# Optimization experiments

Hardware: AMD Instinct MI355X
Metric: run time of the kernel (lower is better)

Reference implementation:

```python
import jax, jax.numpy as jnp
import numpy as np
from jax.scipy.special import logsumexp

B, T, LD, HD, K = 64, 2048, 16, 64, 8
TEMP = 1.0  # annealing=False
LOG2PI = float(np.log(2.0 * np.pi))


def setup_inputs() -> dict:
    key = jax.random.key(0)
    ks = jax.random.split(key, 10)
    return {
        "z": jax.random.normal(ks[0], (B, T, LD), jnp.float32),
        "pi": jax.random.normal(ks[1], (K,), jnp.float32) * 0.5,
        "Q": jax.random.normal(ks[2], (K, K), jnp.float32) * 0.5,
        "init_mean": jax.random.normal(ks[3], (K, LD), jnp.float32),
        # torch init: rand(K,1,1) * eye(LD) * 5  (a scale factor per state)
        "init_cov": jax.random.uniform(ks[4], (K, 1, 1), jnp.float32) * 5.0 * jnp.eye(LD, dtype=jnp.float32)[None],
        "covs": jnp.tile(jnp.eye(LD, dtype=jnp.float32)[None], (K, 1, 1)) + 0.05 * jax.random.normal(ks[5], (K, LD, LD), jnp.float32),
        "W1": jax.random.normal(ks[6], (K, HD, LD), jnp.float32) / np.sqrt(LD),
        "b1": jnp.zeros((K, HD), jnp.float32),
        "W2": jax.random.normal(ks[7], (K, LD, HD), jnp.float32) / np.sqrt(HD),
        "b2": jnp.zeros((K, LD), jnp.float32),
    }


def _chol_terms(C):
    """Sigma = C C^T + 1e-6 I ; return (L^{-1}, 0.5*logdet) per state."""
    dim = C.shape[-1]
    Sigma = C @ jnp.swapaxes(C, -1, -2) + 1e-6 * jnp.eye(dim, dtype=C.dtype)
    L = jnp.linalg.cholesky(Sigma)  # [K,D,D]
    Linv = jax.vmap(lambda l: jax.scipy.linalg.solve_triangular(l, jnp.eye(dim, dtype=C.dtype), lower=True))(L)
    logdet_half = jnp.sum(jnp.log(jnp.diagonal(L, axis1=-2, axis2=-1)), -1)  # [K]
    return Linv, logdet_half


def _mvn_logp(diff, Linv, logdet_half):
    # diff [B,t,K,D], Linv [K,D,D] -> [B,t,K]
    y = jnp.einsum('kde,btke->btkd', Linv, diff)
    maha = jnp.sum(y * y, -1)
    d = diff.shape[-1]
    return -0.5 * maha - logdet_half - 0.5 * d * LOG2PI


def reference(z, pi, Q, init_mean, init_cov, covs, W1, b1, W2, b2):
    # ---- local evidence: log p(z_1|s_1), log p(z_t | z_{t-1}, s_t)  [B,T,K]
    Linv0, ld0 = _chol_terms(init_cov)
    le1 = _mvn_logp(z[:, :1, None, :] - init_mean, Linv0, ld0)  # [B,1,K]
    zp = z[:, :-1]  # [B,T-1,D]
    h = jax.nn.softplus(jnp.einsum('btd,khd->btkh', zp, W1) + b1)  # per-state MLP hidden
    mu = jnp.einsum('btkh,kdh->btkd', h, W2) + b2  # [B,T-1,K,D]
    LinvT, ldT = _chol_terms(covs)
    leT = _mvn_logp(z[:, 1:, None, :] - mu, LinvT, ldT)  # [B,T-1,K]
    le = jnp.concatenate([le1, leT], axis=1)  # [B,T,K]

    # ---- alpha recursion (filtering)
    logpi = jax.nn.log_softmax(pi / TEMP)
    Qlog = jax.nn.log_softmax(Q / TEMP, axis=-1)  # log p(s_t=j | s_{t-1}=i)
    QT = Qlog.T  # [to, from]
    lp0 = le[:, 0] + logpi
    lz0 = logsumexp(lp0, -1)
    la0 = lp0 - lz0[:, None]
    le_rest = jnp.swapaxes(le[:, 1:], 0, 1)  # [T-1,B,K]

    def astep(la_prev, le_t):
        lp = logsumexp(le_t[:, :, None] + QT[None] + la_prev[:, None, :], axis=-1)
        lz = logsumexp(lp, -1)
        la = lp - lz[:, None]
        return la, (la, lz)

    _, (las, lzs) = jax.lax.scan(astep, la0, le_rest)
    log_alpha = jnp.concatenate([la0[:, None], jnp.swapaxes(las, 0, 1)], axis=1)  # [B,T,K]
    log_Z = jnp.concatenate([lz0[:, None], lzs.T], axis=1)  # [B,T]

    # ---- beta recursion (smoothing), reverse scan
    def bstep(lb_next, inp):
        le_t, lz_t = inp
        lb = logsumexp(Qlog[None] + le_t[:, None, :] + lb_next[:, None, :], axis=-1) - lz_t[:, None]
        return lb, lb

    _, lbs = jax.lax.scan(bstep, jnp.zeros((B, K), le.dtype), (le_rest, log_Z[:, 1:].T), reverse=True)
    log_beta = jnp.concatenate([jnp.swapaxes(lbs, 0, 1), jnp.zeros((B, 1, K), le.dtype)], axis=1)

    # ---- posteriors
    gamma = jnp.exp(log_alpha + log_beta)  # [B,T,K]
    paired = jnp.exp(Qlog[None, None] + log_alpha[:, :-1, :, None] + log_beta[:, 1:, None, :] + le[:, 1:, None, :] - log_Z[:, 1:, None, None])  # [B,T-1,K,K]
    return gamma, paired, log_Z
```

## Files before the change

### kernel.cpp

```cpp
#include <hip/hip_runtime.h>

#define B_ 64
#define T_ 2048
#define LD_ 16
#define HD_ 64
#define K_ 8
#define L_ 8
#define C_ 256
#define S_ 32

constexpr int OFF_LE    = 0;
constexpr int OFF_ALPHA = 1048576;
constexpr int OFF_ZT    = OFF_ALPHA;
constexpr int OFF_SBUF  = 2097152;
constexpr int OFF_UBUF  = 2228224;
constexpr int OFF_RLOG  = 2359296;
constexpr int OFF_ULOG  = 2375680;
constexpr int OFF_SAIN  = 2377728;
constexpr int OFF_BENT  = 2394112;
constexpr int OFF_PBUF  = 2410496;
constexpr int OFF_PRML  = 3459072;
constexpr int OFF_FRAG  = 3463680;

constexpr int P_LINV0 = 0;
constexpr int P_LINVT = 2048;
constexpr int P_LD0   = 4096;
constexpr int P_LDT   = 4104;
constexpr int P_LOGPI = 4112;

constexpr int FI_NC2 = 32768;
constexpr int FI_C0I = 32896;

constexpr int OUT_PAIRED = B_*T_*K_;
constexpr int OUT_LOGZ   = OUT_PAIRED + B_*(T_-1)*K_*K_;

template<int CTRL>
__device__ __forceinline__ float dppmov(float x) {
  int xi = __float_as_int(x);
  int r = __builtin_amdgcn_update_dpp(xi, xi, CTRL, 0xF, 0xF, true);
  return __int_as_float(r);
}
__device__ __forceinline__ void allg8(float v, float w[8]) {
  w[0] = v;
  w[1] = dppmov<0xB1>(v);
  w[2] = dppmov<0x4E>(v);
  w[3] = dppmov<0x4E>(w[1]);
  w[7] = dppmov<0x141>(v);
  w[6] = dppmov<0xB1>(w[7]);
  w[5] = dppmov<0x4E>(w[7]);
  w[4] = dppmov<0x4E>(w[6]);
}
template<int V> __device__ __forceinline__ float xorg8(float x);
template<> __device__ __forceinline__ float xorg8<0>(float x) { return x; }
template<> __device__ __forceinline__ float xorg8<1>(float x) { return dppmov<0xB1>(x); }
template<> __device__ __forceinline__ float xorg8<2>(float x) { return dppmov<0x4E>(x); }
template<> __device__ __forceinline__ float xorg8<3>(float x) { return dppmov<0x4E>(dppmov<0xB1>(x)); }
template<> __device__ __forceinline__ float xorg8<4>(float x) { return dppmov<0x4E>(dppmov<0xB1>(dppmov<0x141>(x))); }
template<> __device__ __forceinline__ float xorg8<5>(float x) { return dppmov<0x4E>(dppmov<0x141>(x)); }
// ... 22 lines not shown
  w[7] = __int_as_float(__builtin_amdgcn_ds_swizzle(x, 0xF8));
}
__device__ __forceinline__ void col2row(const float cl[8], float rv[8]) {
  rv[0] = cl[0];
  rv[1] = xorg8<1>(cl[1]);
  rv[2] = xorg8<2>(cl[2]);
  rv[3] = xorg8<3>(cl[3]);
  rv[4] = xorg8<4>(cl[4]);
  rv[5] = xorg8<5>(cl[5]);
  rv[6] = xorg8<6>(cl[6]);
  rv[7] = xorg8<7>(cl[7]);
}
__device__ __forceinline__ void mmul8(const float a[8], const float m[8], float o[8]) {
  float m8[8][8];
  #pragma unroll
  for (int w = 0; w < 8; w++) allg8(m[w], m8[w]);
  #pragma unroll
  for (int v = 0; v < 8; v++) {
    float acc = 0.f;
    #pragma unroll
    for (int u = 0; u < 8; u++) acc = __builtin_fmaf(a[u], m8[u^v][u], acc);
    o[v] = acc;
  }
}
__device__ __forceinline__ float maxnorm8(float m[8]) {
  float mx = m[0];
  #pragma unroll
  for (int u = 1; u < 8; u++) mx = fmaxf(mx, m[u]);
  mx = bfly_max8(mx);
  float r = rcpnr(mx);
  #pragma unroll
  for (int u = 0; u < 8; u++) m[u] *= r;
  return mx;
}
__device__ __forceinline__ void load_rows(const float* p, float r[8]) {
  const float4* q = (const float4*)p;
  float4 x0 = q[0], x1 = q[1];
  r[0]=x0.x; r[1]=x0.y; r[2]=x0.z; r[3]=x0.w;
  r[4]=x1.x; r[5]=x1.y; r[6]=x1.z; r[7]=x1.w;
}
__device__ __forceinline__ float dotw8(const float r[8], const float w[8]) {
  return ((r[0]*w[0]+r[1]*w[1]) + (r[2]*w[2]+r[3]*w[3]))
       + ((r[4]*w[4]+r[5]*w[5]) + (r[6]*w[6]+r[7]*w[7]));
}
__device__ __forceinline__ void fill_Qe(const float* __restrict__ Qm, float* Qe) {
  if (threadIdx.x < 8) {
    int r = threadIdx.x;
    float qq[8], mx = -1e30f;
    #pragma unroll
    for (int c2 = 0; c2 < 8; c2++) { qq[c2] = Qm[r*8+c2]; mx = fmaxf(mx, qq[c2]); }
    float s = 0.f;
    #pragma unroll
    for (int c2 = 0; c2 < 8; c2++) s += __expf(qq[c2]-mx);
    float ls = __logf(s);
    #pragma unroll
    for (int c2 = 0; c2 < 8; c2++) Qe[r*8+c2] = __expf(qq[c2]-mx-ls);
  }
}

typedef __attribute__((ext_vector_type(4))) float f32x4;
typedef __attribute__((ext_vector_type(8))) short bf16x8;

__device__ __forceinline__ unsigned ph(float a, float b) {
  return (__float_as_uint(a) >> 16) | (__float_as_uint(b) & 0xFFFF0000u);
}
__device__ __forceinline__ float hif(float a) {
  return __uint_as_float(__float_as_uint(a) & 0xFFFF0000u);
}
__device__ __forceinline__ bf16x8 u2f(uint4 u) {
  return __builtin_bit_cast(bf16x8, u);
}
__device__ __forceinline__ uint4 mkfrag_u4(float4 v) {
  unsigned ux = __float_as_uint(v.x), uy = __float_as_uint(v.y);
  unsigned uz = __float_as_uint(v.z), uw = __float_as_uint(v.w);
  unsigned h01 = (ux >> 16) | (uy & 0xFFFF0000u);
  unsigned h23 = (uz >> 16) | (uw & 0xFFFF0000u);
  float lx = v.x - __uint_as_float(ux & 0xFFFF0000u);
  float ly = v.y - __uint_as_float(uy & 0xFFFF0000u);
  float lz = v.z - __uint_as_float(uz & 0xFFFF0000u);
  float lw = v.w - __uint_as_float(uw & 0xFFFF0000u);
  return make_uint4(h01, h23, ph(lx,ly), ph(lz,lw));
}
__device__ __forceinline__ f32x4 MF(bf16x8 a, bf16x8 b, f32x4 c) {
  return __builtin_amdgcn_mfma_f32_16x16x32_bf16(a, b, c, 0, 0, 0);
}

__global__ __launch_bounds__(64) void prep_kernel(
    const float* __restrict__ pi, const float* __restrict__ Q,
    const float* __restrict__ init_cov, const float* __restrict__ covs,
    float* __restrict__ prm)
{
  int tid = threadIdx.x;
  int blk = blockIdx.x;
  if (blk < 16) {
    int k = blk & 7;
    const float* C = (blk < 8 ? init_cov : covs) + k*256;
    float* outL  = prm + (blk < 8 ? P_LINV0 : P_LINVT) + k*256;
    float* outld = prm + (blk < 8 ? P_LD0   : P_LDT)   + k;
    __shared__ float S[16][17], L[16][17], X[16][17];
    for (int e = tid; e < 256; e += 64) {
      int r = e >> 4, c = e & 15;
      float s = (r == c) ? 1e-6f : 0.f;
      for (int l = 0; l < 16; l++) s += C[r*16+l] * C[c*16+l];
      S[r][c] = s;
    }
    __syncthreads();
    for (int j = 0; j < 16; j++) {
      if (tid == 0) L[j][j] = sqrtf(S[j][j]);
      __syncthreads();
      if (tid > j && tid < 16) L[tid][j] = S[tid][j] / L[j][j];
      __syncthreads();
      if (tid > j && tid < 16) {
        float ltj = L[tid][j];
        for (int c = j+1; c <= tid; c++) S[tid][c] -= ltj * L[c][j];
      }
      __syncthreads();
    }
    if (tid < 16) {
      int c = tid;
      for (int r = 0; r < 16; r++) {
        float v;
        if (r < c) v = 0.f;
        else {
          v = (r == c) ? 1.f : 0.f;
          for (int s2 = c; s2 < r; s2++) v -= L[r][s2] * X[s2][c];
          v /= L[r][r];
        }
        X[r][c] = v;
      }
    }
    __syncthreads();
    for (int e = tid; e < 256; e += 64) outL[e] = X[e>>4][e&15];
    if (tid == 0) {
      float ld = 0.f;
      for (int j = 0; j < 16; j++) ld += logf(L[j][j]);
      *outld = ld;
    }
  } else {
    if (tid == 0) {
      float p[8], mx = -1e30f;
      for (int j = 0; j < 8; j++) { p[j] = pi[j]; mx = fmaxf(mx, p[j]); }
      float s = 0.f;
      for (int j = 0; j < 8; j++) s += __expf(p[j]-mx);
      float ls = logf(s);
      for (int j = 0; j < 8; j++) prm[P_LOGPI+j] = p[j]-mx-ls;
    }
  }
}

__global__ __launch_bounds__(64) void prep2_kernel(
    const float* __restrict__ W1, const float* __restrict__ W2,
    const float* __restrict__ b2, const float* __restrict__ init_mean,
    const float* __restrict__ prm, float* __restrict__ frag)
{
  int k = blockIdx.x, tid = threadIdx.x;
  __shared__ float Ls[16][16], L0s[16][16], G[16][64];
  for (int e = tid; e < 256; e += 64) {
    Ls[e>>4][e&15]  = prm[P_LINVT + k*256 + e];
    L0s[e>>4][e&15] = prm[P_LINV0 + k*256 + e];
  }
  __syncthreads();
  for (int idx = tid; idx < 1024; idx += 64) {
    int d = idx >> 6, hh = idx & 63;
    float s = 0.f;
    for (int e = 0; e < 16; e++) s += Ls[d][e] * W2[k*1024 + e*64 + hh];
    G[d][hh] = -s;
  }
  __syncthreads();
  int d = tid & 15, q = tid >> 4;
  uint4* F4 = (uint4*)frag;
  for (int kc = 0; kc < 2; kc++) {
    float v[8], lo[8];
    for (int j = 0; j < 8; j++) {
      int hh = 32*kc + 16*(j>>2) + 4*q + (j&3);
      v[j] = G[d][hh];
      lo[j] = v[j] - hif(v[j]);
    }
    F4[6144 + ((k*2+kc)*4+q)*16 + d] =
        make_uint4(ph(v[0],v[1]), ph(v[2],v[3]), ph(v[4],v[5]), ph(v[6],v[7]));
    F4[7168 + ((k*2+kc)*4+q)*16 + d] =
        make_uint4(ph(lo[0],lo[1]), ph(lo[2],lo[3]), ph(lo[4],lo[5]), ph(lo[6],lo[7]));
  }
  for (int mt = 0; mt < 4; mt++) {
    int hh = 16*mt + d;
    float v[4], lo[4];
    for (int j = 0; j < 4; j++) { v[j] = W1[k*1024 + hh*16 + 4*q + j]; lo[j] = v[j] - hif(v[j]); }
    unsigned x = ph(v[0],v[1]), y = ph(v[2],v[3]);
    F4[((k*4+mt)*4+q)*16 + d]        = make_uint4(x, y, x, y);
    F4[2048 + ((k*4+mt)*4+q)*16 + d] = make_uint4(ph(lo[0],lo[1]), ph(lo[2],lo[3]), 0u, 0u);
  }
  {
    float v[4], lo[4];
    for (int j = 0; j < 4; j++) { v[j] = Ls[d][4*q+j]; lo[j] = v[j] - hif(v[j]); }
    unsigned x = ph(v[0],v[1]), y = ph(v[2],v[3]);
    F4[4096 + (k*4+q)*16 + d] = make_uint4(x, y, x, y);
    F4[4608 + (k*4+q)*16 + d] = make_uint4(ph(lo[0],lo[1]), ph(lo[2],lo[3]), 0u, 0u);
    for (int j = 0; j < 4; j++) { v[j] = L0s[d][4*q+j]; lo[j] = v[j] - hif(v[j]); }
    x = ph(v[0],v[1]); y = ph(v[2],v[3]);
    F4[5120 + (k*4+q)*16 + d] = make_uint4(x, y, x, y);
    F4[5632 + (k*4+q)*16 + d] = make_uint4(ph(lo[0],lo[1]), ph(lo[2],lo[3]), 0u, 0u);
  }
  if (q == 0) {
    float s2 = 0.f, s0 = 0.f;
    for (int e = 0; e < 16; e++) {
      s2 += Ls[d][e]  * b2[k*16+e];
      s0 += L0s[d][e] * init_mean[k*16+e];
    }
    frag[FI_NC2 + k*16 + d] = -s2;
    frag[FI_C0I + k*16 + d] = -s0;
  }
}

__global__ __launch_bounds__(256) void ztr_kernel(
    const float* __restrict__ z, uint4* __restrict__ zf)
{
  int tid = blockIdx.x*256 + threadIdx.x;
  int t = tid >> 6, b = tid & 63;
  const float4* src = (const float4*)(z + (b*T_ + t)*LD_);
  #pragma unroll
  for (int q = 0; q < 4; q++)
    zf[(t*4 + q)*64 + b] = mkfrag_u4(src[q]);
}

__global__ __launch_bounds__(256) void emisB_kernel(
    const uint4* __restrict__ zf, const float* __restrict__ b1,
    const float* __restrict__ frag, const float* __restrict__ prm,
    float* __restrict__ lebuf)
{
  int lane = threadIdx.x & 63;
  int wid = __builtin_amdgcn_readfirstlane(blockIdx.x*4 + (threadIdx.x >> 6));
  int bblk = wid & 3;
  int tch  = (wid >> 2) & 255;
  int k    = wid >> 10;
  int c = lane & 15, q = lane >> 4;
  int b = bblk*16 + c;
  const uint4* F4 = (const uint4*)frag;

  bf16x8 w1a1[4], w1a2[4];
  #pragma unroll
  for (int mt = 0; mt < 4; mt++) {
    w1a1[mt] = u2f(F4[((k*4+mt)*4+q)*16 + c]);
    w1a2[mt] = u2f(F4[2048 + ((k*4+mt)*4+q)*16 + c]);
// ... 3 lines not shown
  bf16x8 gahi[2], galo[2];
  #pragma unroll
  for (int kc = 0; kc < 2; kc++) {
    gahi[kc] = u2f(F4[6144 + ((k*2+kc)*4+q)*16 + c]);
    galo[kc] = u2f(F4[7168 + ((k*2+kc)*4+q)*16 + c]);
  }
  float b1iv[16];
  #pragma unroll
  for (int i = 0; i < 16; i++)
    b1iv[i] = b1[k*64 + (i>>2)*16 + 4*q + (i&3)];
  float nc2[4];
  #pragma unroll
  for (int r = 0; r < 4; r++) nc2[r] = frag[FI_NC2 + k*16 + 4*q + r];
  float lconst = -prm[P_LDT + k] - 14.70301653f;

  int t0 = tch*8;
  bf16x8 zp;
  int ttstart;
  if (tch == 0) {
    bf16x8 zc0 = u2f(zf[q*64 + b]);
    bf16x8 l0a1 = u2f(F4[5120 + (k*4+q)*16 + c]);
    bf16x8 l0a2 = u2f(F4[5632 + (k*4+q)*16 + c]);
    f32x4 acc;
    acc[0] = frag[FI_C0I + k*16 + 4*q + 0];
    acc[1] = frag[FI_C0I + k*16 + 4*q + 1];
    acc[2] = frag[FI_C0I + k*16 + 4*q + 2];
    acc[3] = frag[FI_C0I + k*16 + 4*q + 3];
    acc = MF(l0a1, zc0, acc);
    acc = MF(l0a2, zc0, acc);
    float m2 = (acc[0]*acc[0] + acc[1]*acc[1]) + (acc[2]*acc[2] + acc[3]*acc[3]);
    m2 += __shfl_xor(m2, 16);
    m2 += __shfl_xor(m2, 32);
    float le = -0.5f*m2 - prm[P_LD0+k] - 14.70301653f + prm[P_LOGPI+k];
    if (q == 0) lebuf[k*64 + b] = le;
    zp = zc0;
    ttstart = 1;
  } else {
    zp = u2f(zf[((t0-1)*4 + q)*64 + b]);
    ttstart = 0;
  }

  uint4 zvu = zf[((t0+ttstart)*4 + q)*64 + b];
  #pragma unroll 1
  for (int tt = ttstart; tt < 8; tt++) {
    int t = t0 + tt;
    uint4 zvn = zvu;
    if (tt < 7) zvn = zf[((t+1)*4 + q)*64 + b];
    bf16x8 zc = u2f(zvu);
    f32x4 a1[4];
    #pragma unroll
    for (int mt = 0; mt < 4; mt++) {
      f32x4 ai;
      ai[0] = b1iv[mt*4+0]; ai[1] = b1iv[mt*4+1];
      ai[2] = b1iv[mt*4+2]; ai[3] = b1iv[mt*4+3];
      ai = MF(w1a1[mt], zp, ai);
      a1[mt] = MF(w1a2[mt], zp, ai);
    }
    float hv[16];
    #pragma unroll
    for (int i = 0; i < 16; i++) {
      float a = a1[i>>2][i&3];
      hv[i] = __logf(1.f + __expf(a));
    }
    bf16x8 hhi[2], hlo[2];
    #pragma unroll
    for (int kc = 0; kc < 2; kc++) {
      const float* hp = hv + 8*kc;
      hhi[kc] = u2f(make_uint4(ph(hp[0],hp[1]), ph(hp[2],hp[3]),
                               ph(hp[4],hp[5]), ph(hp[6],hp[7])));
      float l0 = hp[0]-hif(hp[0]), l1 = hp[1]-hif(hp[1]);
      float l2 = hp[2]-hif(hp[2]), l3 = hp[3]-hif(hp[3]);
      float l4 = hp[4]-hif(hp[4]), l5 = hp[5]-hif(hp[5]);
      float l6 = hp[6]-hif(hp[6]), l7 = hp[7]-hif(hp[7]);
      hlo[kc] = u2f(make_uint4(ph(l0,l1), ph(l2,l3), ph(l4,l5), ph(l6,l7)));
    }
    f32x4 acc;
    acc[0] = nc2[0]; acc[1] = nc2[1]; acc[2] = nc2[2]; acc[3] = nc2[3];
    acc = MF(lva1, zc, acc);
    acc = MF(lva2, zc, acc);
    #pragma unroll
    for (int kc = 0; kc < 2; kc++) {
      acc = MF(gahi[kc], hhi[kc], acc);
      acc = MF(galo[kc], hhi[kc], acc);
      acc = MF(gahi[kc], hlo[kc], acc);
    }
    float m2 = (acc[0]*acc[0] + acc[1]*acc[1]) + (acc[2]*acc[2] + acc[3]*acc[3]);
    m2 += __shfl_xor(m2, 16);
    m2 += __shfl_xor(m2, 32);
    float le = -0.5f*m2 + lconst;
    if (q == 0) lebuf[t*512 + k*64 + b] = le;
    zp = zc;
    zvu = zvn;
  }
}

__global__ __launch_bounds__(256) void fwdA_kernel(
    const float* __restrict__ lebuf, const float* __restrict__ Qm,
    float* __restrict__ pbuf, float* __restrict__ sbuf)
{
  __shared__ float Qe[64];
  __shared__ float M[4][8][64];
  fill_Qe(Qm, Qe);
  int lane64 = threadIdx.x & 63;
  int iu = threadIdx.x >> 6;
  int unit = blockIdx.x*4 + iu;
  int b = unit & 63, s = unit >> 6;
  int u = lane64 >> 3, j = lane64 & 7;
  int c = 8*s + u;
  float lev[8];
  #pragma unroll
  for (int x = 0; x < 8; x++) lev[x] = lebuf[(c*L_+x)*512 + j*64 + b];
  __syncthreads();
  float qtv[64];
  #pragma unroll
  for (int x = 0; x < 8; x++)
    #pragma unroll
    for (int v = 0; v < 8; v++)
      qtv[x*8+v] = Qe[(j^v)*8 + (j^x)];
  float pl[8];
  if (c == 0) {
    float m = bfly_max8(lev[0]);
    float e = __expf(lev[0]-m);
    allg8(e, pl);
  } else {
    float m = bfly_max8(lev[0]);
    float e = __expf(lev[0]-m);
    float e8[8]; allg8(e, e8);
    float np[8];
    #pragma unroll
    for (int x = 0; x < 8; x++) np[x] = e8[x] * qtv[x*8];
    float mx = np[0];
    #pragma unroll
    for (int x = 1; x < 8; x++) mx = fmaxf(mx, np[x]);
    mx = bfly_max8(mx);
    float r = rcpnr(mx);
    #pragma unroll
    for (int x = 0; x < 8; x++) pl[x] = np[x] * r;
  }
  #pragma unroll
  for (int sx = 1; sx < 8; sx++) {
    float m = bfly_max8(lev[sx]);
    float e = __expf(lev[sx]-m);
    float e8[8]; allg8(e, e8);
    float np[8];
    #pragma unroll
    for (int x = 0; x < 8; x++) {
      float acc = 0.f;
      #pragma unroll
      for (int v = 0; v < 8; v++) acc = __builtin_fmaf(qtv[x*8+v], pl[v], acc);
      np[x] = e8[x] * acc;
    }
    float mx = np[0];
    #pragma unroll
    for (int x = 1; x < 8; x++) mx = fmaxf(mx, np[x]);
    mx = bfly_max8(mx);
    float r = rcpnr(mx);
    #pragma unroll
    for (int x = 0; x < 8; x++) pl[x] = np[x] * r;
  }
  float rv[8]; col2row(pl, rv);
  float4* dst = (float4*)(pbuf + (c*64 + b)*64 + j*8);
  dst[0] = make_float4(rv[0], rv[1], rv[2], rv[3]);
  dst[1] = make_float4(rv[4], rv[5], rv[6], rv[7]);
  #pragma unroll
  for (int v = 0; v < 8; v++) M[iu][u][j*8+v] = rv[v];
  __syncthreads();
  if (u == 0) {
    float m[8];
    #pragma unroll
    for (int v = 0; v < 8; v++) m[v] = M[iu][0][j*8+v];
    for (int cc = 1; cc < 8; cc++) {
      float a[8];
      #pragma unroll
      for (int v = 0; v < 8; v++) a[v] = M[iu][cc][j*8+v];
      float nm[8];
      mmul8(a, m, nm);
      maxnorm8(nm);
      #pragma unroll
      for (int v = 0; v < 8; v++) m[v] = nm[v];
    }
    float4* d2 = (float4*)(sbuf + (s*64 + b)*64 + j*8);
    d2[0] = make_float4(m[0], m[1], m[2], m[3]);
    d2[1] = make_float4(m[4], m[5], m[6], m[7]);
  }
}

__global__ __launch_bounds__(512) void fwdP2b_kernel(
    const float* __restrict__ sbuf, float* __restrict__ sain)
{
  int lane = threadIdx.x;
  int b = lane >> 3, i = lane & 7;
  const float4* base = (const float4*)sbuf;
  float4 c0 = base[(0*64+b)*16 + i*2], c1 = base[(0*64+b)*16 + i*2 + 1];
  float a = 0.125f;
  for (int s = 0; s < S_; s++) {
    int s2 = (s < S_-1) ? s+1 : S_-1;
    float4 n0 = base[(s2*64+b)*16 + i*2], n1 = base[(s2*64+b)*16 + i*2 + 1];
    float aw[8]; allg8(a, aw);
    float sm = ((c0.x*aw[0] + c0.y*aw[1]) + (c0.z*aw[2] + c0.w*aw[3]))
             + ((c1.x*aw[4] + c1.y*aw[5]) + (c1.z*aw[6] + c1.w*aw[7]));
    float tot = bfly_sum8(sm);
    float an = sm * rcpnr(tot);
    if (s < S_-1) { a = an; sain[(s+1)*512 + b*8 + i] = a; }
    c0 = n0; c1 = n1;
  }
}

__global__ __launch_bounds__(256) void fwdB_kernel(
    const float* __restrict__ lebuf, const float* __restrict__ Qm,
    const float* __restrict__ sain, float* pbuf,
    float* __restrict__ alpha, float* __restrict__ rlog,
    float* __restrict__ ubuf, float* __restrict__ ulog,
    float* __restrict__ out)
{
  __shared__ float Qe[64];
  __shared__ float Als[4][8];
  __shared__ float Mh[4][8][64];
  __shared__ float Lh[4][8];
  fill_Qe(Qm, Qe);
  int lane64 = threadIdx.x & 63;
  int iu = threadIdx.x >> 6;
  int unit = blockIdx.x*4 + iu;
  int b = unit & 63, s = unit >> 6;
  int u = lane64 >> 3, i = lane64 & 7;
  int c = 8*s + u;
  int off = b*8 + i;
  float pr[8];
  load_rows(pbuf + (c*64 + b)*64 + i*8, pr);
  float lev[8];
  #pragma unroll
  for (int x = 0; x < 8; x++) lev[x] = lebuf[(c*L_+x)*512 + i*64 + b];
  __syncthreads();
  float q[8];
  #pragma unroll
  for (int x = 0; x < 8; x++) q[x] = Qe[(i^x)*8 + i];
  float av_in = 0.f;
  if (u == 0) av_in = (s == 0) ? 0.125f : sain[s*512 + off];
  for (int r = 0; r < 7; r++) {
    if (u == r) {
      if (r > 0) av_in = Als[iu][i];
      float aw[8]; allg8(av_in, aw);
      float sm = dotw8(pr, aw);
      float tot = bfly_sum8(sm);
      Als[iu][i] = sm * rcpnr(tot);
    }
    __syncthreads();
  }
  if (u == 7) av_in = Als[iu][i];
  float* logZ = out + OUT_LOGZ + b*T_;
  float eb_loc[8];
  float a;
  if (c == 0) {
    float m0 = bfly_max8(lev[0]);
    float e0x = __expf(lev[0]-m0);
    float ct = bfly_sum8(e0x);
    float rr = rcpnr(ct);
    a = e0x * rr;
    alpha[off] = a;
    eb_loc[0] = a;
    if (i == 0) logZ[0] = m0 + __logf(ct);
  } else {
    a = av_in;
    int t = c*L_;
    float m = bfly_max8(lev[0]);
    float e = __expf(lev[0]-m);
    float w[8]; allg8(a, w);
    float dot = dotw8(q, w);
    float p = e * dot;
    float ct = bfly_sum8(p);
    float rr = rcpnr(ct);
    a = p * rr;
    alpha[t*512 + off] = a;
    eb_loc[0] = e * rr;
    if (i == 0) logZ[t] = m + __logf(ct);
  }
  #pragma unroll
  for (int x = 1; x < 8; x++) {
    int t = c*L_ + x;
    float m = bfly_max8(lev[x]);
    float e = __expf(lev[x]-m);
    float w[8]; allg8(a, w);
    float dot = dotw8(q, w);
    float p = e * dot;
    float ct = bfly_sum8(p);
    float rr = rcpnr(ct);
    a = p * rr;
    alpha[t*512 + off] = a;
    eb_loc[x] = e * rr;
    if (i == 0) logZ[t] = m + __logf(ct);
  }
  float qv[64];
  #pragma unroll
  for (int x = 0; x < 8; x++)
    #pragma unroll
    for (int v = 0; v < 8; v++)
      qv[x*8+v] = Qe[(i^x)*8 + (i^v)];
  float rl8[8];
  #pragma unroll
  for (int x = 0; x < 8; x++) rl8[x] = (x == 0) ? 1.f : 0.f;
  float lsc = 0.f;
  #pragma unroll
  for (int sx = 7; sx >= 1; sx--) {
    float e8[8]; allg8(eb_loc[sx], e8);
    float nr[8];
    #pragma unroll
    for (int x = 0; x < 8; x++) {
      float acc = 0.f;
      #pragma unroll
      for (int v = 0; v < 8; v++) acc = __builtin_fmaf(qv[x*8+v], e8[v]*rl8[v], acc);
      nr[x] = acc;
    }
    float mx = nr[0];
    #pragma unroll
    for (int x = 1; x < 8; x++) mx = fmaxf(mx, nr[x]);
    mx = bfly_max8(mx);
    float r = rcpnr(mx);
    #pragma unroll
    for (int x = 0; x < 8; x++) rl8[x] = nr[x] * r;
    lsc += __logf(mx);
  }
  float rv[8]; col2row(rl8, rv);
  float4* dstR = (float4*)(pbuf + (c*64 + b)*64 + i*8);
  dstR[0] = make_float4(rv[0], rv[1], rv[2], rv[3]);
  dstR[1] = make_float4(rv[4], rv[5], rv[6], rv[7]);
  if (i == 0) rlog[c*64 + b] = lsc;
  float qr[8];
  #pragma unroll
  for (int x = 0; x < 8; x++) qr[x] = Qe[i*8 + (i^x)];
  float d8[8];
  #pragma unroll
  for (int v = 0; v < 8; v++) d8[v] = eb_loc[0] * rv[v];
  float h8[8];
  mmul8(qr, d8, h8);
  float ls = lsc + __logf(maxnorm8(h8));
  #pragma unroll
  for (int v = 0; v < 8; v++) Mh[iu][u][i*8+v] = h8[v];
  if (i == 0) Lh[iu][u] = ls;
  __syncthreads();
  if (u == 0) {
    float m[8];
    #pragma unroll
    for (int v = 0; v < 8; v++) m[v] = Mh[iu][7][i*8+v];
    float lsum = Lh[iu][7];
    for (int cc = 6; cc >= 0; cc--) {
      float aa[8];
      #pragma unroll
      for (int v = 0; v < 8; v++) aa[v] = Mh[iu][cc][i*8+v];
      float t8[8];
      mmul8(aa, m, t8);
      lsum += Lh[iu][cc] + __logf(maxnorm8(t8));
      #pragma unroll
      for (int v = 0; v < 8; v++) m[v] = t8[v];
    }
    float4* d2 = (float4*)(ubuf + (s*64 + b)*64 + i*8);
    d2[0] = make_float4(m[0], m[1], m[2], m[3]);
    d2[1] = make_float4(m[4], m[5], m[6], m[7]);
    if (i == 0) ulog[s*64 + b] = lsum;
  }
}

__global__ __launch_bounds__(512) void bwdP2b_kernel(
    const float* __restrict__ ubuf, const float* __restrict__ ulog,
    float* __restrict__ bent)
{
  int lane = threadIdx.x;
  int b = lane >> 3, i = lane & 7;
  bent[(S_-1)*512 + b*8 + i] = 1.f;
  const float4* base = (const float4*)ubuf;
  float sh = 1.f, sig = 0.f;
  float4 c0 = base[((S_-1)*64+b)*16 + i*2], c1 = base[((S_-1)*64+b)*16 + i*2 + 1];
  float cu = ulog[(S_-1)*64 + b];
  for (int s = S_-1; s >= 1; s--) {
    int s2 = (s > 1) ? s-1 : 1;
    float4 n0 = base[(s2*64+b)*16 + i*2], n1 = base[(s2*64+b)*16 + i*2 + 1];
    float nu = ulog[s2*64 + b];
    float sw[8]; allg8(sh, sw);
    float y = ((c0.x*sw[0] + c0.y*sw[1]) + (c0.z*sw[2] + c0.w*sw[3]))
            + ((c1.x*sw[4] + c1.y*sw[5]) + (c1.z*sw[6] + c1.w*sw[7]));
    float mx = bfly_max8(y);
    sh = y * rcpnr(mx);
    sig += cu + __logf(mx);
    bent[(s-1)*512 + b*8 + i] = sh * __expf(sig);
    c0 = n0; c1 = n1; cu = nu;
  }
}

__global__ __launch_bounds__(256) void bwdC_kernel(
    const float* __restrict__ alpha, const float* __restrict__ lebuf,
    const float* __restrict__ rbuf, const float* __restrict__ rlog,
    const float* __restrict__ Qm, const float* __restrict__ bent,
    float* __restrict__ out)
{
  __shared__ float Qe[64];
  __shared__ float Bls[4][8];
  fill_Qe(Qm, Qe);
  int lane64 = threadIdx.x & 63;
  int iu = threadIdx.x >> 6;
  int unit = blockIdx.x*4 + iu;
  int b = unit & 63, s = unit >> 6;
  int u = lane64 >> 3, i = lane64 & 7;
  int c = 8*s + u;
  int off = b*8 + i;
  float r8[8];
  load_rows(rbuf + (c*64 + b)*64 + i*8, r8);
  float erl = __expf(rlog[c*64 + b]);
  float av[8], lev[8];
  #pragma unroll
  for (int x = 0; x < 8; x++) av[x] = alpha[(c*L_+x)*512 + off];
  #pragma unroll
  for (int x = 0; x < 8; x++) lev[x] = lebuf[(c*L_+x)*512 + i*64 + b];
  const float* lzp = out + OUT_LOGZ + b*T_ + c*L_;
  float4 lz0 = *(const float4*)lzp;
  float4 lz1 = *(const float4*)(lzp + 4);
  float ev[8];
  ev[0] = __expf(lev[0]-lz0.x); ev[1] = __expf(lev[1]-lz0.y);
  ev[2] = __expf(lev[2]-lz0.z); ev[3] = __expf(lev[3]-lz0.w);
  ev[4] = __expf(lev[4]-lz1.x); ev[5] = __expf(lev[5]-lz1.y);
  ev[6] = __expf(lev[6]-lz1.z); ev[7] = __expf(lev[7]-lz1.w);
  float e0 = ev[0];
  float avm1 = (c > 0) ? alpha[(c*L_-1)*512 + off] : 0.f;
  __syncthreads();
  float qr[8], qa[8];
  #pragma unroll
  for (int x = 0; x < 8; x++) qr[x] = Qe[i*8 + (i^x)];
  #pragma unroll
  for (int v = 0; v < 8; v++) qa[v] = Qe[i*8 + v];
  float bt = 0.f, y = 0.f, nbv = 0.f;
  for (int r = 7; r >= 0; r--) {
    if (u == r) {
      bt = (r == 7) ? bent[s*512 + off] : Bls[iu][i];
      float bw[8]; allg8(bt, bw);
      y = dotw8(r8, bw) * erl;
      float ey = e0 * y;
      float w[8]; allg8(ey, w);
      nbv = 0.f;
      #pragma unroll
      for (int v = 0; v < 8; v++) nbv = __builtin_fmaf(qr[v], w[v], nbv);
      if (r > 0) Bls[iu][i] = nbv;
    }
    __syncthreads();
  }
  float* po = out + OUT_PAIRED + b*((T_-1)*64);
  float* go = out + b*(T_*K_);
  float bb = bt;
  if (c == C_-1) go[2047*8 + i] = av[7];
  #pragma unroll
  for (int x = 7; x >= 1; x--) {
    float eya[8]; absg8(ev[x]*bb, eya);
    float term[8];
    #pragma unroll
    for (int v = 0; v < 8; v++) term[v] = qa[v]*eya[v];
    float nb = ((term[0]+term[1]) + (term[2]+term[3]))
             + ((term[4]+term[5]) + (term[6]+term[7]));
    int t = c*L_ + x - 1;
    float am = av[x-1];
    float4* pd = (float4*)(po + t*64 + i*8);
    pd[0] = make_float4(am*term[0], am*term[1], am*term[2], am*term[3]);
    pd[1] = make_float4(am*term[4], am*term[5], am*term[6], am*term[7]);
    go[t*8 + i] = am*nb;
    bb = nb;
  }
  if (c > 0) {
    float eya[8]; absg8(e0*y, eya);
    int t = c*L_ - 1;
    float4* pd = (float4*)(po + t*64 + i*8);
    pd[0] = make_float4(avm1*qa[0]*eya[0], avm1*qa[1]*eya[1],
                        avm1*qa[2]*eya[2], avm1*qa[3]*eya[3]);
    pd[1] = make_float4(avm1*qa[4]*eya[4], avm1*qa[5]*eya[5],
                        avm1*qa[6]*eya[6], avm1*qa[7]*eya[7]);
    go[t*8 + i] = avm1 * nbv;
  }
}

extern "C" void kernel_launch(void* const* d_in, const int* in_sizes, int n_in,
                              void* d_out, int out_size, void* d_ws, size_t ws_size,
                              hipStream_t stream) {
  const float* z         = (const float*)d_in[0];
  const float* pi        = (const float*)d_in[1];
  const float* Q         = (const float*)d_in[2];
  const float* init_mean = (const float*)d_in[3];
  const float* init_cov  = (const float*)d_in[4];
  const float* covs      = (const float*)d_in[5];
  const float* W1        = (const float*)d_in[6];
  const float* b1        = (const float*)d_in[7];
  const float* W2        = (const float*)d_in[8];
  const float* b2        = (const float*)d_in[9];
  float* out = (float*)d_out;
  float* ws  = (float*)d_ws;

  prep_kernel<<<17, 64, 0, stream>>>(pi, Q, init_cov, covs, ws + OFF_PRML);
  prep2_kernel<<<8, 64, 0, stream>>>(W1, W2, b2, init_mean, ws + OFF_PRML,
                                     ws + OFF_FRAG);
  ztr_kernel<<<512, 256, 0, stream>>>(z, (uint4*)(ws + OFF_ZT));
  emisB_kernel<<<2048, 256, 0, stream>>>((const uint4*)(ws + OFF_ZT), b1,
                                         ws + OFF_FRAG, ws + OFF_PRML,
                                         ws + OFF_LE);
  fwdA_kernel<<<512, 256, 0, stream>>>(ws + OFF_LE, Q, ws + OFF_PBUF,
                                       ws + OFF_SBUF);
  fwdP2b_kernel<<<1, 512, 0, stream>>>(ws + OFF_SBUF, ws + OFF_SAIN);
  fwdB_kernel<<<512, 256, 0, stream>>>(ws + OFF_LE, Q, ws + OFF_SAIN,
                                       ws + OFF_PBUF, ws + OFF_ALPHA,
                                       ws + OFF_RLOG, ws + OFF_UBUF,
                                       ws + OFF_ULOG, out);
  bwdP2b_kernel<<<1, 512, 0, stream>>>(ws + OFF_UBUF, ws + OFF_ULOG,
                                       ws + OFF_BENT);
  bwdC_kernel<<<512, 256, 0, stream>>>(ws + OFF_ALPHA, ws + OFF_LE,
                                       ws + OFF_PBUF, ws + OFF_RLOG, Q,
                                       ws + OFF_BENT, out);
}
```

Before: 234.1 us.

## Halve chunk length, recompute chunk transfer matrices instead of staging through pbuf

Chunk length drops from 8 to 4 steps, so there are twice as many chunks and superchunks and the fwdA/fwdB/bwdC grids double. The per-chunk forward and backward transfer matrices are no longer written to and reloaded from a global pbuf/rlog buffer. fwdB and bwdC now recompute them locally from the emissions. The serial superchunk scan kernels become fully unrolled direct loads over a longer sequence of 64 steps. This trades global memory traffic and a longer serial pass for redundant in-register compute and more parallel work.

```diff
diff --git a/kernel.cpp b/kernel.cpp
--- a/kernel.cpp
+++ b/kernel.cpp
@@ -5,22 +5,20 @@
 #define LD_ 16
 #define HD_ 64
 #define K_ 8
-#define L_ 8
-#define C_ 256
-#define S_ 32
+#define L_ 4
+#define C_ 512
+#define S_ 64
 
 constexpr int OFF_LE    = 0;
 constexpr int OFF_ALPHA = 1048576;
 constexpr int OFF_ZT    = OFF_ALPHA;
 constexpr int OFF_SBUF  = 2097152;
-constexpr int OFF_UBUF  = 2228224;
-constexpr int OFF_RLOG  = 2359296;
-constexpr int OFF_ULOG  = 2375680;
-constexpr int OFF_SAIN  = 2377728;
-constexpr int OFF_BENT  = 2394112;
-constexpr int OFF_PBUF  = 2410496;
-constexpr int OFF_PRML  = 3459072;
-constexpr int OFF_FRAG  = 3463680;
+constexpr int OFF_UBUF  = 2359296;
+constexpr int OFF_ULOG  = 2621440;
+constexpr int OFF_SAIN  = 2625536;
+constexpr int OFF_BENT  = 2658304;
+constexpr int OFF_PRML  = 3145728;
+constexpr int OFF_FRAG  = 3150336;
 
 constexpr int P_LINV0 = 0;
 constexpr int P_LINVT = 2048;
@@ -112,12 +110,6 @@
   #pragma unroll
   for (int u = 0; u < 8; u++) m[u] *= r;
   return mx;
-}
-__device__ __forceinline__ void load_rows(const float* p, float r[8]) {
-  const float4* q = (const float4*)p;
-  float4 x0 = q[0], x1 = q[1];
-  r[0]=x0.x; r[1]=x0.y; r[2]=x0.z; r[3]=x0.w;
-  r[4]=x1.x; r[5]=x1.y; r[6]=x1.z; r[7]=x1.w;
 }
 __device__ __forceinline__ float dotw8(const float r[8], const float w[8]) {
   return ((r[0]*w[0]+r[1]*w[1]) + (r[2]*w[2]+r[3]*w[3]))
@@ -421,7 +413,7 @@
 
 __global__ __launch_bounds__(256) void fwdA_kernel(
     const float* __restrict__ lebuf, const float* __restrict__ Qm,
-    float* __restrict__ pbuf, float* __restrict__ sbuf)
+    float* __restrict__ sbuf)
 {
   __shared__ float Qe[64];
   __shared__ float M[4][8][64];
@@ -432,9 +424,9 @@
   int b = unit & 63, s = unit >> 6;
   int u = lane64 >> 3, j = lane64 & 7;
   int c = 8*s + u;
-  float lev[8];
-  #pragma unroll
-  for (int x = 0; x < 8; x++) lev[x] = lebuf[(c*L_+x)*512 + j*64 + b];
+  float lev[L_];
+  #pragma unroll
+  for (int x = 0; x < L_; x++) lev[x] = lebuf[(c*L_+x)*512 + j*64 + b];
   __syncthreads();
   float qtv[64];
   #pragma unroll
@@ -463,7 +455,7 @@
     for (int x = 0; x < 8; x++) pl[x] = np[x] * r;
   }
   #pragma unroll
-  for (int sx = 1; sx < 8; sx++) {
+  for (int sx = 1; sx < L_; sx++) {
     float m = bfly_max8(lev[sx]);
     float e = __expf(lev[sx]-m);
     float e8[8]; allg8(e, e8);
@@ -484,9 +476,6 @@
     for (int x = 0; x < 8; x++) pl[x] = np[x] * r;
   }
   float rv[8]; col2row(pl, rv);
-  float4* dst = (float4*)(pbuf + (c*64 + b)*64 + j*8);
-  dst[0] = make_float4(rv[0], rv[1], rv[2], rv[3]);
-  dst[1] = make_float4(rv[4], rv[5], rv[6], rv[7]);
   #pragma unroll
   for (int v = 0; v < 8; v++) M[iu][u][j*8+v] = rv[v];
   __syncthreads();
@@ -516,25 +505,23 @@
   int lane = threadIdx.x;
   int b = lane >> 3, i = lane & 7;
   const float4* base = (const float4*)sbuf;
-  float4 c0 = base[(0*64+b)*16 + i*2], c1 = base[(0*64+b)*16 + i*2 + 1];
   float a = 0.125f;
-  for (int s = 0; s < S_; s++) {
-    int s2 = (s < S_-1) ? s+1 : S_-1;
-    float4 n0 = base[(s2*64+b)*16 + i*2], n1 = base[(s2*64+b)*16 + i*2 + 1];
+  #pragma unroll
+  for (int s = 0; s < S_-1; s++) {
+    float4 c0 = base[(s*64+b)*16 + i*2];
+    float4 c1 = base[(s*64+b)*16 + i*2 + 1];
     float aw[8]; allg8(a, aw);
     float sm = ((c0.x*aw[0] + c0.y*aw[1]) + (c0.z*aw[2] + c0.w*aw[3]))
              + ((c1.x*aw[4] + c1.y*aw[5]) + (c1.z*aw[6] + c1.w*aw[7]));
     float tot = bfly_sum8(sm);
-    float an = sm * rcpnr(tot);
-    if (s < S_-1) { a = an; sain[(s+1)*512 + b*8 + i] = a; }
-    c0 = n0; c1 = n1;
+    a = sm * rcpnr(tot);
+    sain[(s+1)*512 + b*8 + i] = a;
   }
 }
 
 __global__ __launch_bounds__(256) void fwdB_kernel(
     const float* __restrict__ lebuf, const float* __restrict__ Qm,
-    const float* __restrict__ sain, float* pbuf,
-    float* __restrict__ alpha, float* __restrict__ rlog,
+    const float* __restrict__ sain, float* __restrict__ alpha,
     float* __restrict__ ubuf, float* __restrict__ ulog,
     float* __restrict__ out)
 {
@@ -550,15 +537,61 @@
   int u = lane64 >> 3, i = lane64 & 7;
   int c = 8*s + u;
   int off = b*8 + i;
+  float lev[L_];
+  #pragma unroll
+  for (int x = 0; x < L_; x++) lev[x] = lebuf[(c*L_+x)*512 + i*64 + b];
+  __syncthreads();
   float pr[8];
-  load_rows(pbuf + (c*64 + b)*64 + i*8, pr);
-  float lev[8];
-  #pragma unroll
-  for (int x = 0; x < 8; x++) lev[x] = lebuf[(c*L_+x)*512 + i*64 + b];
-  __syncthreads();
-  float q[8];
-  #pragma unroll
-  for (int x = 0; x < 8; x++) q[x] = Qe[(i^x)*8 + i];
+  {
+    float qtv[64];
+    #pragma unroll
+    for (int x = 0; x < 8; x++)
+      #pragma unroll
+      for (int v = 0; v < 8; v++)
+        qtv[x*8+v] = Qe[(i^v)*8 + (i^x)];
+    float pl[8];
+    if (c == 0) {
+      float m = bfly_max8(lev[0]);
+      float e = __expf(lev[0]-m);
+      allg8(e, pl);
+    } else {
+      float m = bfly_max8(lev[0]);
+      float e = __expf(lev[0]-m);
+      float e8[8]; allg8(e, e8);
+      float np[8];
+      #pragma unroll
+      for (int x = 0; x < 8; x++) np[x] = e8[x] * qtv[x*8];
+      float mx = np[0];
+      #pragma unroll
+      for (int x = 1; x < 8; x++) mx = fmaxf(mx, np[x]);
+      mx = bfly_max8(mx);
+      float r = rcpnr(mx);
+      #pragma unroll
+      for (int x = 0; x < 8; x++) pl[x] = np[x] * r;
+    }
+    #pragma unroll
+    for (int sx = 1; sx < L_; sx++) {
+      float m = bfly_max8(lev[sx]);
+      float e = __expf(lev[sx]-m);
+      float e8[8]; allg8(e, e8);
+      float np[8];
+      #pragma unroll
+      for (int x = 0; x < 8; x++) {
+        float acc = 0.f;
+        #pragma unroll
+        for (int v = 0; v < 8; v++) acc = __builtin_fmaf(qtv[x*8+v], pl[v], acc);
+        np[x] = e8[x] * acc;
+      }
+      float mx = np[0];
+      #pragma unroll
+      for (int x = 1; x < 8; x++) mx = fmaxf(mx, np[x]);
+      mx = bfly_max8(mx);
+      float r = rcpnr(mx);
+      #pragma unroll
+      for (int x = 0; x < 8; x++) pl[x] = np[x] * r;
+    }
+    col2row(pl, pr);
+  }
   float av_in = 0.f;
   if (u == 0) av_in = (s == 0) ? 0.125f : sain[s*512 + off];
   for (int r = 0; r < 7; r++) {
@@ -572,8 +605,11 @@
     __syncthreads();
   }
   if (u == 7) av_in = Als[iu][i];
+  float q[8];
+  #pragma unroll
+  for (int x = 0; x < 8; x++) q[x] = Qe[(i^x)*8 + i];
   float* logZ = out + OUT_LOGZ + b*T_;
-  float eb_loc[8];
+  float eb_loc[L_];
   float a;
   if (c == 0) {
     float m0 = bfly_max8(lev[0]);
@@ -600,7 +636,7 @@
     if (i == 0) logZ[t] = m + __logf(ct);
   }
   #pragma unroll
-  for (int x = 1; x < 8; x++) {
+  for (int x = 1; x < L_; x++) {
     int t = c*L_ + x;
     float m = bfly_max8(lev[x]);
     float e = __expf(lev[x]-m);
@@ -614,41 +650,40 @@
     eb_loc[x] = e * rr;
     if (i == 0) logZ[t] = m + __logf(ct);
   }
-  float qv[64];
-  #pragma unroll
-  for (int x = 0; x < 8; x++)
-    #pragma unroll
-    for (int v = 0; v < 8; v++)
-      qv[x*8+v] = Qe[(i^x)*8 + (i^v)];
-  float rl8[8];
-  #pragma unroll
-  for (int x = 0; x < 8; x++) rl8[x] = (x == 0) ? 1.f : 0.f;
+  float rv[8];
   float lsc = 0.f;
-  #pragma unroll
-  for (int sx = 7; sx >= 1; sx--) {
-    float e8[8]; allg8(eb_loc[sx], e8);
-    float nr[8];
-    #pragma unroll
-    for (int x = 0; x < 8; x++) {
-      float acc = 0.f;
-      #pragma unroll
-      for (int v = 0; v < 8; v++) acc = __builtin_fmaf(qv[x*8+v], e8[v]*rl8[v], acc);
-      nr[x] = acc;
-    }
-    float mx = nr[0];
-    #pragma unroll
-    for (int x = 1; x < 8; x++) mx = fmaxf(mx, nr[x]);
-    mx = bfly_max8(mx);
-    float r = rcpnr(mx);
-    #pragma unroll
-    for (int x = 0; x < 8; x++) rl8[x] = nr[x] * r;
-    lsc += __logf(mx);
-  }
-  float rv[8]; col2row(rl8, rv);
-  float4* dstR = (float4*)(pbuf + (c*64 + b)*64 + i*8);
-  dstR[0] = make_float4(rv[0], rv[1], rv[2], rv[3]);
-  dstR[1] = make_float4(rv[4], rv[5], rv[6], rv[7]);
-  if (i == 0) rlog[c*64 + b] = lsc;
+  {
+    float qv[64];
+    #pragma unroll
+    for (int x = 0; x < 8; x++)
+      #pragma unroll
+      for (int v = 0; v < 8; v++)
+        qv[x*8+v] = Qe[(i^x)*8 + (i^v)];
+    float rl8[8];
+    #pragma unroll
+    for (int x = 0; x < 8; x++) rl8[x] = (x == 0) ? 1.f : 0.f;
+    #pragma unroll
+    for (int sx = L_-1; sx >= 1; sx--) {
+      float e8[8]; allg8(eb_loc[sx], e8);
+      float nr[8];
+      #pragma unroll
+      for (int x = 0; x < 8; x++) {
+        float acc = 0.f;
+        #pragma unroll
+        for (int v = 0; v < 8; v++) acc = __builtin_fmaf(qv[x*8+v], e8[v]*rl8[v], acc);
+        nr[x] = acc;
+      }
+      float mx = nr[0];
+      #pragma unroll
+      for (int x = 1; x < 8; x++) mx = fmaxf(mx, nr[x]);
+      mx = bfly_max8(mx);
+      float r = rcpnr(mx);
+      #pragma unroll
+      for (int x = 0; x < 8; x++) rl8[x] = nr[x] * r;
+      lsc += __logf(mx);
+    }
+    col2row(rl8, rv);
+  }
   float qr[8];
   #pragma unroll
   for (int x = 0; x < 8; x++) qr[x] = Qe[i*8 + (i^x)];
@@ -693,12 +728,11 @@
   bent[(S_-1)*512 + b*8 + i] = 1.f;
   const float4* base = (const float4*)ubuf;
   float sh = 1.f, sig = 0.f;
-  float4 c0 = base[((S_-1)*64+b)*16 + i*2], c1 = base[((S_-1)*64+b)*16 + i*2 + 1];
-  float cu = ulog[(S_-1)*64 + b];
+  #pragma unroll
   for (int s = S_-1; s >= 1; s--) {
-    int s2 = (s > 1) ? s-1 : 1;
-    float4 n0 = base[(s2*64+b)*16 + i*2], n1 = base[(s2*64+b)*16 + i*2 + 1];
-    float nu = ulog[s2*64 + b];
+    float4 c0 = base[(s*64+b)*16 + i*2];
+    float4 c1 = base[(s*64+b)*16 + i*2 + 1];
+    float cu = ulog[s*64 + b];
     float sw[8]; allg8(sh, sw);
     float y = ((c0.x*sw[0] + c0.y*sw[1]) + (c0.z*sw[2] + c0.w*sw[3]))
             + ((c1.x*sw[4] + c1.y*sw[5]) + (c1.z*sw[6] + c1.w*sw[7]));
@@ -706,13 +740,11 @@
     sh = y * rcpnr(mx);
     sig += cu + __logf(mx);
     bent[(s-1)*512 + b*8 + i] = sh * __expf(sig);
-    c0 = n0; c1 = n1; cu = nu;
   }
 }
 
 __global__ __launch_bounds__(256) void bwdC_kernel(
     const float* __restrict__ alpha, const float* __restrict__ lebuf,
-    const float* __restrict__ rbuf, const float* __restrict__ rlog,
     const float* __restrict__ Qm, const float* __restrict__ bent,
     float* __restrict__ out)
 {
@@ -726,22 +758,15 @@
   int u = lane64 >> 3, i = lane64 & 7;
   int c = 8*s + u;
   int off = b*8 + i;
-  float r8[8];
-  load_rows(rbuf + (c*64 + b)*64 + i*8, r8);
-  float erl = __expf(rlog[c*64 + b]);
-  float av[8], lev[8];
-  #pragma unroll
-  for (int x = 0; x < 8; x++) av[x] = alpha[(c*L_+x)*512 + off];
-  #pragma unroll
-  for (int x = 0; x < 8; x++) lev[x] = lebuf[(c*L_+x)*512 + i*64 + b];
-  const float* lzp = out + OUT_LOGZ + b*T_ + c*L_;
-  float4 lz0 = *(const float4*)lzp;
-  float4 lz1 = *(const float4*)(lzp + 4);
-  float ev[8];
-  ev[0] = __expf(lev[0]-lz0.x); ev[1] = __expf(lev[1]-lz0.y);
-  ev[2] = __expf(lev[2]-lz0.z); ev[3] = __expf(lev[3]-lz0.w);
-  ev[4] = __expf(lev[4]-lz1.x); ev[5] = __expf(lev[5]-lz1.y);
-  ev[6] = __expf(lev[6]-lz1.z); ev[7] = __expf(lev[7]-lz1.w);
+  float av[L_], lev[L_];
+  #pragma unroll
+  for (int x = 0; x < L_; x++) av[x] = alpha[(c*L_+x)*512 + off];
+  #pragma unroll
+  for (int x = 0; x < L_; x++) lev[x] = lebuf[(c*L_+x)*512 + i*64 + b];
+  float4 lz = *(const float4*)(out + OUT_LOGZ + b*T_ + c*L_);
+  float ev[L_];
+  ev[0] = __expf(lev[0]-lz.x); ev[1] = __expf(lev[1]-lz.y);
+  ev[2] = __expf(lev[2]-lz.z); ev[3] = __expf(lev[3]-lz.w);
   float e0 = ev[0];
   float avm1 = (c > 0) ? alpha[(c*L_-1)*512 + off] : 0.f;
   __syncthreads();
@@ -750,6 +775,42 @@
   for (int x = 0; x < 8; x++) qr[x] = Qe[i*8 + (i^x)];
   #pragma unroll
   for (int v = 0; v < 8; v++) qa[v] = Qe[i*8 + v];
+  float r8[8];
+  float erl;
+  {
+    float qv[64];
+    #pragma unroll
+    for (int x = 0; x < 8; x++)
+      #pragma unroll
+      for (int v = 0; v < 8; v++)
+        qv[x*8+v] = Qe[(i^x)*8 + (i^v)];
+    float rl8[8];
+    #pragma unroll
+    for (int x = 0; x < 8; x++) rl8[x] = (x == 0) ? 1.f : 0.f;
+    float lsc = 0.f;
+    #pragma unroll
+    for (int sx = L_-1; sx >= 1; sx--) {
+      float e8[8]; allg8(ev[sx], e8);
+      float nr[8];
+      #pragma unroll
+      for (int x = 0; x < 8; x++) {
+        float acc = 0.f;
+        #pragma unroll
+        for (int v = 0; v < 8; v++) acc = __builtin_fmaf(qv[x*8+v], e8[v]*rl8[v], acc);
+        nr[x] = acc;
+      }
+      float mx = nr[0];
+      #pragma unroll
+      for (int x = 1; x < 8; x++) mx = fmaxf(mx, nr[x]);
+      mx = bfly_max8(mx);
+      float r = rcpnr(mx);
+      #pragma unroll
+      for (int x = 0; x < 8; x++) rl8[x] = nr[x] * r;
+      lsc += __logf(mx);
+    }
+    col2row(rl8, r8);
+    erl = __expf(lsc);
+  }
   float bt = 0.f, y = 0.f, nbv = 0.f;
   for (int r = 7; r >= 0; r--) {
     if (u == r) {
@@ -768,9 +829,9 @@
   float* po = out + OUT_PAIRED + b*((T_-1)*64);
   float* go = out + b*(T_*K_);
   float bb = bt;
-  if (c == C_-1) go[2047*8 + i] = av[7];
-  #pragma unroll
-  for (int x = 7; x >= 1; x--) {
+  if (c == C_-1) go[2047*8 + i] = av[L_-1];
+  #pragma unroll
+  for (int x = L_-1; x >= 1; x--) {
     float eya[8]; absg8(ev[x]*bb, eya);
     float term[8];
     #pragma unroll
@@ -820,16 +881,13 @@
   emisB_kernel<<<2048, 256, 0, stream>>>((const uint4*)(ws + OFF_ZT), b1,
                                          ws + OFF_FRAG, ws + OFF_PRML,
                                          ws + OFF_LE);
-  fwdA_kernel<<<512, 256, 0, stream>>>(ws + OFF_LE, Q, ws + OFF_PBUF,
-                                       ws + OFF_SBUF);
+  fwdA_kernel<<<1024, 256, 0, stream>>>(ws + OFF_LE, Q, ws + OFF_SBUF);
   fwdP2b_kernel<<<1, 512, 0, stream>>>(ws + OFF_SBUF, ws + OFF_SAIN);
-  fwdB_kernel<<<512, 256, 0, stream>>>(ws + OFF_LE, Q, ws + OFF_SAIN,
-                                       ws + OFF_PBUF, ws + OFF_ALPHA,
-                                       ws + OFF_RLOG, ws + OFF_UBUF,
-                                       ws + OFF_ULOG, out);
+  fwdB_kernel<<<1024, 256, 0, stream>>>(ws + OFF_LE, Q, ws + OFF_SAIN,
+                                        ws + OFF_ALPHA, ws + OFF_UBUF,
+                                        ws + OFF_ULOG, out);
   bwdP2b_kernel<<<1, 512, 0, stream>>>(ws + OFF_UBUF, ws + OFF_ULOG,
                                        ws + OFF_BENT);
-  bwdC_kernel<<<512, 256, 0, stream>>>(ws + OFF_ALPHA, ws + OFF_LE,
-                                       ws + OFF_PBUF, ws + OFF_RLOG, Q,
-                                       ws + OFF_BENT, out);
-}
+  bwdC_kernel<<<1024, 256, 0, stream>>>(ws + OFF_ALPHA, ws + OFF_LE, Q,
+                                        ws + OFF_BENT, out);
+}
```

Result: slower. 241.9 us (+3.3%).

## Merge prep kernels and transpose emission buffer to chunk-major rows

Applied to the files above, without the earlier changes.

Folds the Cholesky/inverse prep kernel and the fragment-building prep kernel into one launch: each block computes both Cholesky factors in shared memory and uses them directly. The emission log-likelihood buffer is re-laid out so that each (chunk, batch, state) owns 8 contiguous time values, letting the forward and backward kernels read them with vectorized row loads instead of 8 strided scalar loads. The cost is scattered 4-byte writes in the emission kernel and serialized Cholesky work inside each prep block.

```diff
diff --git a/kernel.cpp b/kernel.cpp
--- a/kernel.cpp
+++ b/kernel.cpp
@@ -22,8 +22,6 @@
 constexpr int OFF_PRML  = 3459072;
 constexpr int OFF_FRAG  = 3463680;
 
-constexpr int P_LINV0 = 0;
-constexpr int P_LINVT = 2048;
 constexpr int P_LD0   = 4096;
 constexpr int P_LDT   = 4104;
 constexpr int P_LOGPI = 4112;
@@ -165,80 +163,64 @@
   return __builtin_amdgcn_mfma_f32_16x16x32_bf16(a, b, c, 0, 0, 0);
 }
 
-__global__ __launch_bounds__(64) void prep_kernel(
-    const float* __restrict__ pi, const float* __restrict__ Q,
-    const float* __restrict__ init_cov, const float* __restrict__ covs,
-    float* __restrict__ prm)
+__device__ void chol16(const float* __restrict__ C,
+                       float S[16][17], float L[16][17], float X[16][17],
+                       float* __restrict__ ldout, int tid)
 {
-  int tid = threadIdx.x;
-  int blk = blockIdx.x;
-  if (blk < 16) {
-    int k = blk & 7;
-    const float* C = (blk < 8 ? init_cov : covs) + k*256;
-    float* outL  = prm + (blk < 8 ? P_LINV0 : P_LINVT) + k*256;
-    float* outld = prm + (blk < 8 ? P_LD0   : P_LDT)   + k;
-    __shared__ float S[16][17], L[16][17], X[16][17];
-    for (int e = tid; e < 256; e += 64) {
-      int r = e >> 4, c = e & 15;
-      float s = (r == c) ? 1e-6f : 0.f;
-      for (int l = 0; l < 16; l++) s += C[r*16+l] * C[c*16+l];
-      S[r][c] = s;
-    }
+  for (int e = tid; e < 256; e += 64) {
+    int r = e >> 4, c = e & 15;
+    float s = (r == c) ? 1e-6f : 0.f;
+    for (int l = 0; l < 16; l++) s += C[r*16+l] * C[c*16+l];
+    S[r][c] = s;
+  }
+  __syncthreads();
+  for (int j = 0; j < 16; j++) {
+    if (tid == 0) L[j][j] = sqrtf(S[j][j]);
     __syncthreads();
-    for (int j = 0; j < 16; j++) {
-      if (tid == 0) L[j][j] = sqrtf(S[j][j]);
-      __syncthreads();
-      if (tid > j && tid < 16) L[tid][j] = S[tid][j] / L[j][j];
-      __syncthreads();
-      if (tid > j && tid < 16) {
-        float ltj = L[tid][j];
-        for (int c = j+1; c <= tid; c++) S[tid][c] -= ltj * L[c][j];
+    if (tid > j && tid < 16) L[tid][j] = S[tid][j] / L[j][j];
+    __syncthreads();
+    if (tid > j && tid < 16) {
+      float ltj = L[tid][j];
+      for (int c = j+1; c <= tid; c++) S[tid][c] -= ltj * L[c][j];
+    }
+    __syncthreads();
+  }
+  if (tid < 16) {
+    int c = tid;
+    for (int r = 0; r < 16; r++) {
+      float v;
+      if (r < c) v = 0.f;
+      else {
+        v = (r == c) ? 1.f : 0.f;
+        for (int s2 = c; s2 < r; s2++) v -= L[r][s2] * X[s2][c];
+        v /= L[r][r];
       }
-      __syncthreads();
-    }
-    if (tid < 16) {
-      int c = tid;
-      for (int r = 0; r < 16; r++) {
-        float v;
-        if (r < c) v = 0.f;
-        else {
-          v = (r == c) ? 1.f : 0.f;
-          for (int s2 = c; s2 < r; s2++) v -= L[r][s2] * X[s2][c];
-          v /= L[r][r];
-        }
-        X[r][c] = v;
-      }
-    }
-    __syncthreads();
-    for (int e = tid; e < 256; e += 64) outL[e] = X[e>>4][e&15];
-    if (tid == 0) {
-      float ld = 0.f;
-      for (int j = 0; j < 16; j++) ld += logf(L[j][j]);
-      *outld = ld;
-    }
-  } else {
-    if (tid == 0) {
-      float p[8], mx = -1e30f;
-      for (int j = 0; j < 8; j++) { p[j] = pi[j]; mx = fmaxf(mx, p[j]); }
-      float s = 0.f;
-      for (int j = 0; j < 8; j++) s += __expf(p[j]-mx);
-      float ls = logf(s);
-      for (int j = 0; j < 8; j++) prm[P_LOGPI+j] = p[j]-mx-ls;
-    }
-  }
-}
-
-__global__ __launch_bounds__(64) void prep2_kernel(
-    const float* __restrict__ W1, const float* __restrict__ W2,
-    const float* __restrict__ b2, const float* __restrict__ init_mean,
-    const float* __restrict__ prm, float* __restrict__ frag)
+      X[r][c] = v;
+    }
+  }
+  if (tid == 0) {
+    float ld = 0.f;
+    for (int j = 0; j < 16; j++) ld += logf(L[j][j]);
+    *ldout = ld;
+  }
+  __syncthreads();
+}
+
+__global__ __launch_bounds__(64) void prepAll_kernel(
+    const float* __restrict__ pi, const float* __restrict__ init_cov,
+    const float* __restrict__ covs, const float* __restrict__ W1,
+    const float* __restrict__ W2, const float* __restrict__ b2,
+    const float* __restrict__ init_mean, float* __restrict__ prm,
+    float* __restrict__ frag)
 {
   int k = blockIdx.x, tid = threadIdx.x;
+  __shared__ float S[16][17], L[16][17], X[16][17];
   __shared__ float Ls[16][16], L0s[16][16], G[16][64];
-  for (int e = tid; e < 256; e += 64) {
-    Ls[e>>4][e&15]  = prm[P_LINVT + k*256 + e];
-    L0s[e>>4][e&15] = prm[P_LINV0 + k*256 + e];
-  }
+  chol16(init_cov + k*256, S, L, X, prm + P_LD0 + k, tid);
+  for (int e = tid; e < 256; e += 64) L0s[e>>4][e&15] = X[e>>4][e&15];
+  __syncthreads();
+  chol16(covs + k*256, S, L, X, prm + P_LDT + k, tid);
+  for (int e = tid; e < 256; e += 64) Ls[e>>4][e&15] = X[e>>4][e&15];
   __syncthreads();
   for (int idx = tid; idx < 1024; idx += 64) {
     int d = idx >> 6, hh = idx & 63;
@@ -288,6 +270,14 @@
     }
     frag[FI_NC2 + k*16 + d] = -s2;
     frag[FI_C0I + k*16 + d] = -s0;
+  }
+  if (k == 0 && tid == 0) {
+    float p[8], mx = -1e30f;
+    for (int j = 0; j < 8; j++) { p[j] = pi[j]; mx = fmaxf(mx, p[j]); }
+    float s = 0.f;
+    for (int j = 0; j < 8; j++) s += __expf(p[j]-mx);
+    float ls = logf(s);
+    for (int j = 0; j < 8; j++) prm[P_LOGPI+j] = p[j]-mx-ls;
   }
 }
 
@@ -357,7 +347,7 @@
     m2 += __shfl_xor(m2, 16);
     m2 += __shfl_xor(m2, 32);
     float le = -0.5f*m2 - prm[P_LD0+k] - 14.70301653f + prm[P_LOGPI+k];
-    if (q == 0) lebuf[k*64 + b] = le;
+    if (q == 0) lebuf[(b*8 + k)*8] = le;
     zp = zc0;
     ttstart = 1;
   } else {
@@ -413,7 +403,7 @@
     m2 += __shfl_xor(m2, 16);
     m2 += __shfl_xor(m2, 32);
     float le = -0.5f*m2 + lconst;
-    if (q == 0) lebuf[t*512 + k*64 + b] = le;
+    if (q == 0) lebuf[(((t>>3)*64 + b)*8 + k)*8 + (t&7)] = le;
     zp = zc;
     zvu = zvn;
   }
@@ -433,8 +423,7 @@
   int u = lane64 >> 3, j = lane64 & 7;
   int c = 8*s + u;
   float lev[8];
-  #pragma unroll
-  for (int x = 0; x < 8; x++) lev[x] = lebuf[(c*L_+x)*512 + j*64 + b];
+  load_rows(lebuf + ((c*64 + b)*8 + j)*8, lev);
   __syncthreads();
   float qtv[64];
   #pragma unroll
@@ -553,8 +542,7 @@
   float pr[8];
   load_rows(pbuf + (c*64 + b)*64 + i*8, pr);
   float lev[8];
-  #pragma unroll
-  for (int x = 0; x < 8; x++) lev[x] = lebuf[(c*L_+x)*512 + i*64 + b];
+  load_rows(lebuf + ((c*64 + b)*8 + i)*8, lev);
   __syncthreads();
   float q[8];
   #pragma unroll
@@ -732,8 +720,7 @@
   float av[8], lev[8];
   #pragma unroll
   for (int x = 0; x < 8; x++) av[x] = alpha[(c*L_+x)*512 + off];
-  #pragma unroll
-  for (int x = 0; x < 8; x++) lev[x] = lebuf[(c*L_+x)*512 + i*64 + b];
+  load_rows(lebuf + ((c*64 + b)*8 + i)*8, lev);
   const float* lzp = out + OUT_LOGZ + b*T_ + c*L_;
   float4 lz0 = *(const float4*)lzp;
   float4 lz1 = *(const float4*)(lzp + 4);
@@ -813,9 +800,8 @@
   float* out = (float*)d_out;
   float* ws  = (float*)d_ws;
 
-  prep_kernel<<<17, 64, 0, stream>>>(pi, Q, init_cov, covs, ws + OFF_PRML);
-  prep2_kernel<<<8, 64, 0, stream>>>(W1, W2, b2, init_mean, ws + OFF_PRML,
-                                     ws + OFF_FRAG);
+  prepAll_kernel<<<8, 64, 0, stream>>>(pi, init_cov, covs, W1, W2, b2,
+                                       init_mean, ws + OFF_PRML, ws + OFF_FRAG);
   ztr_kernel<<<512, 256, 0, stream>>>(z, (uint4*)(ws + OFF_ZT));
   emisB_kernel<<<2048, 256, 0, stream>>>((const uint4*)(ws + OFF_ZT), b1,
                                          ws + OFF_FRAG, ws + OFF_PRML,
```

Result: slower. 238.9 us (+2.0%).
